# Optimization experiments

Hardware: AMD Instinct MI355X
Metric: run time of the kernel (lower is better)

The kernel has to match this reference:

```python
import jax, jax.numpy as jnp
import numpy as np

NC, NM, E = 100000, 50000, 1000000
IN_C, IN_M, HID, OUT = 128, 64, 128, 64


def setup_inputs() -> dict:
    key = jax.random.key(0)
    ks = jax.random.split(key, 24)
    f = lambda k, shp: jax.random.normal(k, shp, dtype=jnp.float32) * 0.05
    inp = {
        'x_customer': f(ks[0], (NC, IN_C)),
        'x_merchant': f(ks[1], (NM, IN_M)),
        'W1cm_l': f(ks[2], (IN_C, HID)), 'W1cm_r': f(ks[3], (IN_M, HID)), 'b1_cm': f(ks[4], (HID,)),
        'W1mc_l': f(ks[5], (IN_M, HID)), 'W1mc_r': f(ks[6], (IN_C, HID)), 'b1_mc': f(ks[7], (HID,)),
        'W2cm_l': f(ks[8], (HID, HID)), 'W2cm_r': f(ks[9], (HID, HID)), 'b2_cm': f(ks[10], (HID,)),
        'W2mc_l': f(ks[11], (HID, HID)), 'W2mc_r': f(ks[12], (HID, HID)), 'b2_mc': f(ks[13], (HID,)),
        'Wout': f(ks[14], (HID, OUT)), 'bout': f(ks[15], (OUT,)),
        'ei_cm_src': jax.random.randint(ks[16], (E,), 0, NC, dtype=jnp.int32),
        'ei_cm_dst': jax.random.randint(ks[17], (E,), 0, NM, dtype=jnp.int32),
        'ei_mc_src': jax.random.randint(ks[18], (E,), 0, NM, dtype=jnp.int32),
        'ei_mc_dst': jax.random.randint(ks[19], (E,), 0, NC, dtype=jnp.int32),
    }
    return inp


def _sage(x_src, x_dst, src, dst, Wl, Wr, b, n_dst):
    # PyG SAGEConv: out = lin_l(mean_{j in N(i)} x_j) + lin_r(x_i)
    msg = x_src[src]                                        # [E, d_src] gather
    s = jax.ops.segment_sum(msg, dst, num_segments=n_dst)   # [n_dst, d_src]
    c = jax.ops.segment_sum(jnp.ones((src.shape[0],), x_src.dtype), dst, num_segments=n_dst)
    agg = s / jnp.maximum(c, 1.0)[:, None]                  # mean aggregation
    return agg @ Wl + b + x_dst @ Wr


def reference(x_customer, x_merchant,
              W1cm_l, W1cm_r, b1_cm, W1mc_l, W1mc_r, b1_mc,
              W2cm_l, W2cm_r, b2_cm, W2mc_l, W2mc_r, b2_mc,
              Wout, bout,
              ei_cm_src, ei_cm_dst, ei_mc_src, ei_mc_dst):
    # Layer 1 (bipartite): customer->merchant and merchant->customer; sum-merge is
    # trivial (one edge type per destination node type), then ReLU.
    h_m = jax.nn.relu(_sage(x_customer, x_merchant, ei_cm_src, ei_cm_dst, W1cm_l, W1cm_r, b1_cm, NM))
    h_c = jax.nn.relu(_sage(x_merchant, x_customer, ei_mc_src, ei_mc_dst, W1mc_l, W1mc_r, b1_mc, NC))
    # Layer 2 (hidden -> hidden)
    h_c2 = _sage(h_m, h_c, ei_mc_src, ei_mc_dst, W2mc_l, W2mc_r, b2_mc, NC)
    # Final linear on 'customer' embeddings
    return h_c2 @ Wout + bout
```

## Files before the change

### kernel.cpp

```cpp
#include <hip/hip_runtime.h>

#define NCUST 100000
#define NMERCH 50000
#define NEDGE 1000000
#define NTOT (NCUST + NMERCH)
#define HID 128
#define INC 128
#define INM 64
#define OUTD 64

#define SHIFT 9
#define BUCKW 512
#define NBUCKET ((NTOT + BUCKW - 1) / BUCKW)
#define EPB 4096
#define EPT (EPB / 256)

typedef __attribute__((ext_vector_type(8))) short s8v;
typedef __attribute__((ext_vector_type(4))) float f32x4;

__device__ __forceinline__ void splitpair(float a, float b, uint& hw, uint& lw) {
    uint ua = __float_as_uint(a), ub = __float_as_uint(b);
    uint ha = ua & 0xFFFF0000u, hb = ub & 0xFFFF0000u;
    hw = hb | (ua >> 16);
    float ra = a - __uint_as_float(ha);
    float rb = b - __uint_as_float(hb);
    lw = (__float_as_uint(rb) & 0xFFFF0000u) | (__float_as_uint(ra) >> 16);
}


__global__ __launch_bounds__(256) void bcount_kernel(const int* __restrict__ cm_dst,
                                                     const int* __restrict__ mc_dst,
                                                     int* __restrict__ bcnt) {
    __shared__ int lh[NBUCKET];
    const int t = threadIdx.x;
    for (int i = t; i < NBUCKET; i += 256) lh[i] = 0;
    __syncthreads();
    const int base = blockIdx.x * EPB;
#pragma unroll
    for (int i = 0; i < EPT; ++i) {
        int idx = base + t + i * 256;
        if (idx < NEDGE) {
            atomicAdd(&lh[cm_dst[idx] >> SHIFT], 1);
        } else if (idx < 2 * NEDGE) {
            atomicAdd(&lh[(NMERCH + mc_dst[idx - NEDGE]) >> SHIFT], 1);
        }
    }
    __syncthreads();
    for (int i = t; i < NBUCKET; i += 256) {
        int c = lh[i];
        if (c > 0) atomicAdd(&bcnt[i], c);
    }
}

__global__ __launch_bounds__(512) void scan_buckets_kernel(const int* __restrict__ bcnt,
                                                           int* __restrict__ bbase,
                                                           int* __restrict__ bcur,
                                                           int* __restrict__ ro) {
    __shared__ int sh[512];
    const int t = threadIdx.x;
    int v = (t < NBUCKET) ? bcnt[t] : 0;
    sh[t] = v;
    __syncthreads();
    for (int off = 1; off < 512; off <<= 1) {
        int x = (t >= off) ? sh[t - off] : 0;
        __syncthreads();
        sh[t] += x;
        __syncthreads();
    }
    if (t < NBUCKET) {
        int e = sh[t] - v;
        bbase[t] = e;
        bcur[t] = e;
    }
    if (t == 0) {
        bbase[NBUCKET] = 2 * NEDGE;
        ro[NTOT] = 2 * NEDGE;
    }
}

__global__ __launch_bounds__(256) void bin_kernel(const int* __restrict__ cm_src,
                                                  const int* __restrict__ cm_dst,
                                                  const int* __restrict__ mc_src,
                                                  const int* __restrict__ mc_dst,
                                                  int* __restrict__ bcur,
                                                  int2* __restrict__ pairs) {
    __shared__ int lhist[NBUCKET];
    __shared__ int lbase[NBUCKET];
    __shared__ int loff[NBUCKET];
    const int t = threadIdx.x;
    for (int i = t; i < NBUCKET; i += 256) { lhist[i] = 0; loff[i] = 0; }
    __syncthreads();
    const int base = blockIdx.x * EPB;
    int k_[EPT], s_[EPT];
#pragma unroll
    for (int i = 0; i < EPT; ++i) {
        int idx = base + t + i * 256;
        int key = -1, src = 0;
        if (idx < NEDGE) {
            key = cm_dst[idx];
            src = cm_src[idx];
        } else if (idx < 2 * NEDGE) {
            key = NMERCH + mc_dst[idx - NEDGE];
            src = mc_src[idx - NEDGE];
        }
        k_[i] = key;
        s_[i] = src;
        if (key >= 0) atomicAdd(&lhist[key >> SHIFT], 1);
    }
    __syncthreads();
    for (int b = t; b < NBUCKET; b += 256) {
        int c = lhist[b];
        if (c > 0) lbase[b] = atomicAdd(&bcur[b], c);
    }
    __syncthreads();
#pragma unroll
    for (int i = 0; i < EPT; ++i) {
        if (k_[i] >= 0) {
            int bk = k_[i] >> SHIFT;
            int p = lbase[bk] + atomicAdd(&loff[bk], 1);
            pairs[p] = make_int2(k_[i], s_[i]);
        }
    }
}

__global__ __launch_bounds__(512) void fillb_kernel(const int2* __restrict__ pairs,
                                                    const int* __restrict__ bbase,
                                                    int* __restrict__ ro,
                                                    int* __restrict__ csr) {
    __shared__ int hist[BUCKW];
    __shared__ int cur[BUCKW];
    const int b = blockIdx.x, t = threadIdx.x;
    const int kb = b << SHIFT;
    const int nk = (kb + BUCKW < NTOT) ? BUCKW : (NTOT - kb);
    hist[t] = 0;
    __syncthreads();
    const int start = bbase[b], end = bbase[b + 1];
    for (int i = start + t; i < end; i += 512) atomicAdd(&hist[pairs[i].x - kb], 1);
    __syncthreads();
    int v = hist[t];
    cur[t] = v;
    __syncthreads();
    for (int off = 1; off < 512; off <<= 1) {
        int x = (t >= off) ? cur[t - off] : 0;
        __syncthreads();
        cur[t] += x;
        __syncthreads();
    }
    int pos = start + cur[t] - v;
    if (t < nk) ro[kb + t] = pos;
    cur[t] = pos;
    __syncthreads();
    for (int i = start + t; i < end; i += 512) {
        int2 rec = pairs[i];
        int p = atomicAdd(&cur[rec.x - kb], 1);
        csr[p] = rec.y;
    }
}


__global__ __launch_bounds__(256) void agg_cm_kernel(const float* __restrict__ xc,
                                                     const int* __restrict__ csr,
                                                     const int* __restrict__ ro,
                                                     float* __restrict__ aggm) {
    int node = blockIdx.x * 4 + (threadIdx.x >> 6);
    int lane = threadIdx.x & 63;
    if (node >= NMERCH) return;
    int start = ro[node], end = ro[node + 1];
    float2 a0 = {0.f, 0.f}, a1 = {0.f, 0.f}, a2 = {0.f, 0.f}, a3 = {0.f, 0.f};
    int e = start;
    for (; e + 4 <= end; e += 4) {
        int s0 = csr[e], s1 = csr[e + 1], s2 = csr[e + 2], s3 = csr[e + 3];
        float2 v0 = *(const float2*)(xc + (size_t)s0 * INC + lane * 2);
        float2 v1 = *(const float2*)(xc + (size_t)s1 * INC + lane * 2);
        float2 v2 = *(const float2*)(xc + (size_t)s2 * INC + lane * 2);
        float2 v3 = *(const float2*)(xc + (size_t)s3 * INC + lane * 2);
        a0.x += v0.x; a0.y += v0.y;
        a1.x += v1.x; a1.y += v1.y;
        a2.x += v2.x; a2.y += v2.y;
        a3.x += v3.x; a3.y += v3.y;
    }
    for (; e < end; ++e) {
        int s0 = csr[e];
        float2 v0 = *(const float2*)(xc + (size_t)s0 * INC + lane * 2);
        a0.x += v0.x; a0.y += v0.y;
    }
    int deg = end - start;
    float cnt = (float)(deg > 0 ? deg : 1);
    float2 o;
    o.x = (a0.x + a1.x + a2.x + a3.x) / cnt;
    o.y = (a0.y + a1.y + a2.y + a3.y) / cnt;
    *(float2*)(aggm + (size_t)node * HID + lane * 2) = o;
}

__global__ __launch_bounds__(256) void agg_mc_kernel(const float* __restrict__ xm,
                                                     const float* __restrict__ t2p,
                                                     const int* __restrict__ csr,
                                                     const int* __restrict__ ro,
                                                     float* __restrict__ agg_c,
                                                     float* __restrict__ aggT2) {
    int node = blockIdx.x * 4 + (threadIdx.x >> 6);
    int lane = threadIdx.x & 63;
    if (node >= NCUST) return;
    int start = ro[NMERCH + node], end = ro[NMERCH + node + 1];
    float a0 = 0.f, a1 = 0.f, a2 = 0.f, a3 = 0.f;
    float h0 = 0.f, h1 = 0.f, h2 = 0.f, h3 = 0.f;
    int e = start;
    for (; e + 4 <= end; e += 4) {
        int s0 = csr[e], s1 = csr[e + 1], s2 = csr[e + 2], s3 = csr[e + 3];
        a0 += xm[(size_t)s0 * INM + lane];
        a1 += xm[(size_t)s1 * INM + lane];
        a2 += xm[(size_t)s2 * INM + lane];
        a3 += xm[(size_t)s3 * INM + lane];
        h0 += t2p[(size_t)s0 * OUTD + lane];
        h1 += t2p[(size_t)s1 * OUTD + lane];
        h2 += t2p[(size_t)s2 * OUTD + lane];
        h3 += t2p[(size_t)s3 * OUTD + lane];
    }
    for (; e < end; ++e) {
        int s0 = csr[e];
        a0 += xm[(size_t)s0 * INM + lane];
        h0 += t2p[(size_t)s0 * OUTD + lane];
    }
    int deg = end - start;
    float cnt = (float)(deg > 0 ? deg : 1);
    agg_c[(size_t)node * INM + lane] = (a0 + a1 + a2 + a3) / cnt;
    aggT2[(size_t)node * OUTD + lane] = (h0 + h1 + h2 + h3) / cnt;
}


__global__ __launch_bounds__(64) void small_mm_kernel(const float* __restrict__ Wa,
                                                      const float* __restrict__ Wb,
                                                      float* __restrict__ o) {
    __shared__ float row[128];
    int r = blockIdx.x, j = threadIdx.x;
    for (int k = j; k < 128; k += 64) row[k] = Wa[r * 128 + k];
    __syncthreads();
    float acc = 0.f;
    for (int k = 0; k < 128; ++k) acc = fmaf(row[k], Wb[k * 64 + j], acc);
    o[r * 64 + j] = acc;
}

__global__ void bprime_kernel(const float* __restrict__ b2, const float* __restrict__ Wout,
                              const float* __restrict__ bout, float* __restrict__ bprime) {
    int j = threadIdx.x;
    float acc = bout[j];
    for (int k = 0; k < HID; ++k) acc = fmaf(b2[k], Wout[k * OUTD + j], acc);
    bprime[j] = acc;
}


__global__ __launch_bounds__(256) void wprep_kernel(const float* __restrict__ w0,
                                                    const float* __restrict__ w1,
                                                    const float* __restrict__ w2,
                                                    const float* __restrict__ w3,
                                                    const float* __restrict__ w4,
                                                    const float* __restrict__ w5,
                                                    short* __restrict__ planes) {
    int b = blockIdx.x;
    const float* src;
    int N, kt, hoff, loff;
    if (b < 4)       { src = w0; N = 128; kt = b;      hoff = 0;      loff = 16384; }
    else if (b < 6)  { src = w1; N = 128; kt = b - 4;  hoff = 32768;  loff = 40960; }
    else if (b < 8)  { src = w2; N = 128; kt = b - 6;  hoff = 49152;  loff = 57344; }
    else if (b < 12) { src = w3; N = 128; kt = b - 8;  hoff = 65536;  loff = 81920; }
    else if (b < 16) { src = w4; N = 64;  kt = b - 12; hoff = 98304;  loff = 106496; }
    else             { src = w5; N = 64;  kt = b - 16; hoff = 114688; loff = 122880; }

    for (int slot = threadIdx.x; slot < N * 4; slot += 256) {
        int n = slot % N, kg = slot / N;
        uint hw[4], lw[4];
#pragma unroll
        for (int p = 0; p < 4; ++p) {
            float a = src[(kt * 32 + kg * 8 + 2 * p) * N + n];
            float c = src[(kt * 32 + kg * 8 + 2 * p + 1) * N + n];
            splitpair(a, c, hw[p], lw[p]);
        }
        size_t eoff = (size_t)((kt * 4 + kg) * N + n) * 8;
        *(int4*)&planes[hoff + eoff] = make_int4(hw[0], hw[1], hw[2], hw[3]);
        *(int4*)&planes[loff + eoff] = make_int4(lw[0], lw[1], lw[2], lw[3]);
    }
}


template <int KA, int KB, int NOUT, bool RELU, bool HASBIAS, bool HASADD>
__global__ __launch_bounds__(256) void mfma_gemm(const float* __restrict__ A,
                                                 const float* __restrict__ B,
                                                 const short* __restrict__ WAh,
                                                 const short* __restrict__ WAl,
                                                 const short* __restrict__ WBh,
                                                 const short* __restrict__ WBl,
                                                 const float* __restrict__ bias,
                                                 const float* __restrict__ add,
                                                 float* __restrict__ out, int M) {
    constexpr int NSA = KA / 32, NSB = KB / 32, NS = NSA + NSB;
    constexpr int CBN = NOUT / 32;

    __shared__ int4 AhL[2][512];
    __shared__ int4 AlL[2][512];

    const int t = threadIdx.x;
    const int lane = t & 63;
    const int wv = t >> 6;
    const int wr = wv >> 1;
    const int wc = wv & 1;
    const int rowbase = blockIdx.x * 128;
    const int srow = t >> 1, kh = t & 1;

    float4 pa[4];

    auto gload = [&](int s) {
        const float* src;
        int lda, ks;
        if (s < NSA) { src = A; lda = KA; ks = s * 32; }
        else         { src = B; lda = KB; ks = (s - NSA) * 32; }
        const int grow = rowbase + srow;
        if (grow < M) {
            const float* p = src + (size_t)grow * lda + ks + kh * 16;
            pa[0] = *(const float4*)(p);
            pa[1] = *(const float4*)(p + 4);
            pa[2] = *(const float4*)(p + 8);
            pa[3] = *(const float4*)(p + 12);
        } else {
            pa[0] = pa[1] = pa[2] = pa[3] = make_float4(0.f, 0.f, 0.f, 0.f);
        }
    };

    auto stage = [&](int bb) {
        uint h[8], l[8];
        splitpair(pa[0].x, pa[0].y, h[0], l[0]);
        splitpair(pa[0].z, pa[0].w, h[1], l[1]);
        splitpair(pa[1].x, pa[1].y, h[2], l[2]);
        splitpair(pa[1].z, pa[1].w, h[3], l[3]);
        splitpair(pa[2].x, pa[2].y, h[4], l[4]);
        splitpair(pa[2].z, pa[2].w, h[5], l[5]);
        splitpair(pa[3].x, pa[3].y, h[6], l[6]);
        splitpair(pa[3].z, pa[3].w, h[7], l[7]);
        const int base0 = (2 * kh) * 128 + srow;
        const int base1 = base0 + 128;
        AhL[bb][base0] = make_int4(h[0], h[1], h[2], h[3]);
        AhL[bb][base1] = make_int4(h[4], h[5], h[6], h[7]);
        AlL[bb][base0] = make_int4(l[0], l[1], l[2], l[3]);
        AlL[bb][base1] = make_int4(l[4], l[5], l[6], l[7]);
    };

    f32x4 acc[4][CBN];
#pragma unroll
    for (int rb = 0; rb < 4; ++rb)
#pragma unroll
        for (int cb = 0; cb < CBN; ++cb) acc[rb][cb] = (f32x4){0.f, 0.f, 0.f, 0.f};

    const int kgl = lane >> 4, ln = lane & 15;

    gload(0);
    stage(0);
    for (int s = 0; s < NS; ++s) {
        if (s + 1 < NS) gload(s + 1);
        __syncthreads();
        const short *wph_, *wpl_;
        int wb;
        if (s < NSA) { wph_ = WAh; wpl_ = WAl; wb = s; }
        else         { wph_ = WBh; wpl_ = WBl; wb = s - NSA; }
        const s8v* wph = (const s8v*)wph_;
        const s8v* wpl = (const s8v*)wpl_;
        s8v bh[CBN], bl[CBN];
#pragma unroll
        for (int cb = 0; cb < CBN; ++cb) {
            int n = wc * (NOUT / 2) + cb * 16 + ln;
            int idx = (wb * 4 + kgl) * NOUT + n;
            bh[cb] = wph[idx];
            bl[cb] = wpl[idx];
        }
        const int bb = s & 1;
#pragma unroll
        for (int rb = 0; rb < 4; ++rb) {
            int row = wr * 64 + rb * 16 + ln;
            s8v ah = *(const s8v*)&AhL[bb][kgl * 128 + row];
            s8v al = *(const s8v*)&AlL[bb][kgl * 128 + row];
#pragma unroll
            for (int cb = 0; cb < CBN; ++cb) {
                acc[rb][cb] = __builtin_amdgcn_mfma_f32_16x16x32_bf16(ah, bh[cb], acc[rb][cb], 0, 0, 0);
                acc[rb][cb] = __builtin_amdgcn_mfma_f32_16x16x32_bf16(ah, bl[cb], acc[rb][cb], 0, 0, 0);
                acc[rb][cb] = __builtin_amdgcn_mfma_f32_16x16x32_bf16(al, bh[cb], acc[rb][cb], 0, 0, 0);
            }
        }
        if (s + 1 < NS) stage((s + 1) & 1);
    }

#pragma unroll
    for (int cb = 0; cb < CBN; ++cb) {
        int col = wc * (NOUT / 2) + cb * 16 + ln;
        float bv = HASBIAS ? bias[col] : 0.f;
#pragma unroll
        for (int rb = 0; rb < 4; ++rb) {
#pragma unroll
            for (int i = 0; i < 4; ++i) {
                int grow = rowbase + wr * 64 + rb * 16 + kgl * 4 + i;
                if (grow < M) {
                    float o = acc[rb][cb][i] + bv;
                    if (HASADD) o += add[(size_t)grow * NOUT + col];
                    if (RELU) o = fmaxf(o, 0.f);
                    out[(size_t)grow * NOUT + col] = o;
                }
            }
        }
    }
}


extern "C" void kernel_launch(void* const* d_in, const int* in_sizes, int n_in,
                              void* d_out, int out_size, void* d_ws, size_t ws_size,
                              hipStream_t stream) {
    const float* x_c    = (const float*)d_in[0];
    const float* x_m    = (const float*)d_in[1];
    const float* W1cm_l = (const float*)d_in[2];
    const float* W1cm_r = (const float*)d_in[3];
    const float* b1_cm  = (const float*)d_in[4];
    const float* W1mc_l = (const float*)d_in[5];
    const float* W1mc_r = (const float*)d_in[6];
    const float* b1_mc  = (const float*)d_in[7];
    const float* W2mc_l = (const float*)d_in[11];
    const float* W2mc_r = (const float*)d_in[12];
    const float* b2_mc  = (const float*)d_in[13];
    const float* Wout   = (const float*)d_in[14];
    const float* bout   = (const float*)d_in[15];
    const int* cm_src   = (const int*)d_in[16];
    const int* cm_dst   = (const int*)d_in[17];
    const int* mc_src   = (const int*)d_in[18];
    const int* mc_dst   = (const int*)d_in[19];
    float* out = (float*)d_out;

    char* ws = (char*)d_ws;
    size_t off = 0;
    auto bump = [&](size_t bytes) -> char* {
        off = (off + 255) & ~(size_t)255;
        char* p = ws + off;
        off += bytes;
        return p;
    };
    int* ro       = (int*)bump((size_t)(NTOT + 1) * 4);
    int* bcnt     = (int*)bump((size_t)NBUCKET * 4);
    int* bbase    = (int*)bump((size_t)(NBUCKET + 1) * 4);
    int* bcur     = (int*)bump((size_t)NBUCKET * 4);
    int* csr      = (int*)bump((size_t)2 * NEDGE * 4);
    float* bufA   = (float*)bump((size_t)NCUST * HID * 4);
    float* t2p    = (float*)bump((size_t)NMERCH * OUTD * 4);
    float* agg_c  = (float*)bump((size_t)NCUST * INM * 4);
    float* aggT2  = (float*)bump((size_t)NCUST * OUTD * 4);
    float* h_c    = (float*)bump((size_t)NCUST * HID * 4);
    float* w2ro   = (float*)bump((size_t)HID * OUTD * 4);
    float* w2lo   = (float*)bump((size_t)HID * OUTD * 4);
    float* bpr    = (float*)bump((size_t)OUTD * 4);
    short* planes = (short*)bump((size_t)131072 * 2);

    float* t_agg_m = bufA;
    float* h_m     = bufA + (size_t)NMERCH * HID;
    int2* pairs    = (int2*)h_c;

    small_mm_kernel<<<128, 64, 0, stream>>>(W2mc_r, Wout, w2ro);
    small_mm_kernel<<<128, 64, 0, stream>>>(W2mc_l, Wout, w2lo);
    bprime_kernel<<<1, 64, 0, stream>>>(b2_mc, Wout, bout, bpr);
    wprep_kernel<<<20, 256, 0, stream>>>(W1cm_l, W1cm_r, W1mc_l, W1mc_r, w2ro, w2lo, planes);

    hipMemsetAsync(bcnt, 0, (size_t)NBUCKET * 4, stream);
    bcount_kernel<<<(2 * NEDGE + EPB - 1) / EPB, 256, 0, stream>>>(cm_dst, mc_dst, bcnt);
    scan_buckets_kernel<<<1, 512, 0, stream>>>(bcnt, bbase, bcur, ro);
    bin_kernel<<<(2 * NEDGE + EPB - 1) / EPB, 256, 0, stream>>>(cm_src, cm_dst, mc_src, mc_dst,
                                                                bcur, pairs);
    fillb_kernel<<<NBUCKET, 512, 0, stream>>>(pairs, bbase, ro, csr);

    short* Pcml_h = planes;           short* Pcml_l = planes + 16384;
    short* Pcmr_h = planes + 32768;   short* Pcmr_l = planes + 40960;
    short* Pmcl_h = planes + 49152;   short* Pmcl_l = planes + 57344;
    short* Pmcr_h = planes + 65536;   short* Pmcr_l = planes + 81920;
    short* Pro_h  = planes + 98304;   short* Pro_l  = planes + 106496;
    short* Plo_h  = planes + 114688;  short* Plo_l  = planes + 122880;

    agg_cm_kernel<<<NMERCH / 4, 256, 0, stream>>>(x_c, csr, ro, t_agg_m);
    mfma_gemm<128, 64, 128, true, true, false><<<(NMERCH + 127) / 128, 256, 0, stream>>>(
        t_agg_m, x_m, Pcml_h, Pcml_l, Pcmr_h, Pcmr_l, b1_cm, nullptr, h_m, NMERCH);

    mfma_gemm<128, 0, 64, false, false, false><<<(NMERCH + 127) / 128, 256, 0, stream>>>(
        h_m, nullptr, Plo_h, Plo_l, nullptr, nullptr, nullptr, nullptr, t2p, NMERCH);

    agg_mc_kernel<<<NCUST / 4, 256, 0, stream>>>(x_m, t2p, csr, ro, agg_c, aggT2);

    mfma_gemm<64, 128, 128, true, true, false><<<(NCUST + 127) / 128, 256, 0, stream>>>(
        agg_c, x_c, Pmcl_h, Pmcl_l, Pmcr_h, Pmcr_l, b1_mc, nullptr, h_c, NCUST);

    mfma_gemm<128, 0, 64, false, true, true><<<(NCUST + 127) / 128, 256, 0, stream>>>(
        h_c, nullptr, Pro_h, Pro_l, nullptr, nullptr, bpr, aggT2, out, NCUST);
}
```

Baseline: 462.1 us.

## Gather bf16 copies of node features and interleave merchant rows for aggregation

Converts x_customer to bf16 and packs x_merchant together with the projected layer-2 merchant features into one interleaved 128-wide bf16 row per merchant. Both aggregation kernels then gather half the bytes per edge, and the merchant-to-customer gather reads one contiguous row instead of two separate arrays. This adds two conversion kernels and a bf16 output path in the GEMM. The price is bf16 rounding of the gathered inputs, which may loosen accuracy compared with the previous split-precision fp32 path.

New measurement: 428.8 us. 7.2% less time.

```diff
diff --git a/kernel.cpp b/kernel.cpp
--- a/kernel.cpp
+++ b/kernel.cpp
@@ -25,6 +25,46 @@
     float ra = a - __uint_as_float(ha);
     float rb = b - __uint_as_float(hb);
     lw = (__float_as_uint(rb) & 0xFFFF0000u) | (__float_as_uint(ra) >> 16);
+}
+
+__device__ __forceinline__ uint f2bfbits(float x) {
+    uint u = __float_as_uint(x);
+    return (u + 0x7FFFu + ((u >> 16) & 1u)) >> 16;
+}
+__device__ __forceinline__ uint packbf(float a, float b) {
+    return f2bfbits(a) | (f2bfbits(b) << 16);
+}
+__device__ __forceinline__ float bflo(uint v) { return __uint_as_float(v << 16); }
+__device__ __forceinline__ float bfhi(uint v) { return __uint_as_float(v & 0xFFFF0000u); }
+
+
+__global__ __launch_bounds__(256) void tobf_kernel(const float* __restrict__ in,
+                                                   ushort* __restrict__ outp, int n8) {
+    int i = blockIdx.x * 256 + threadIdx.x;
+    if (i >= n8) return;
+    const float4* p = (const float4*)in + (size_t)i * 2;
+    float4 u = p[0], v = p[1];
+    uint4 w;
+    w.x = packbf(u.x, u.y);
+    w.y = packbf(u.z, u.w);
+    w.z = packbf(v.x, v.y);
+    w.w = packbf(v.z, v.w);
+    ((uint4*)outp)[i] = w;
+}
+
+__global__ __launch_bounds__(256) void xmpack_kernel(const float* __restrict__ xm,
+                                                     ushort* __restrict__ mcpk) {
+    int tid = blockIdx.x * 256 + threadIdx.x;
+    if (tid >= NMERCH * 8) return;
+    int n = tid >> 3, c = (tid & 7) * 8;
+    const float* p = xm + (size_t)n * INM + c;
+    float4 u = *(const float4*)p, v = *(const float4*)(p + 4);
+    uint4 w;
+    w.x = packbf(u.x, u.y);
+    w.y = packbf(u.z, u.w);
+    w.z = packbf(v.x, v.y);
+    w.w = packbf(v.z, v.w);
+    *(uint4*)(mcpk + (size_t)n * 128 + c) = w;
 }
 
 
@@ -158,7 +198,7 @@
 }
 
 
-__global__ __launch_bounds__(256) void agg_cm_kernel(const float* __restrict__ xc,
+__global__ __launch_bounds__(256) void agg_cm_kernel(const ushort* __restrict__ xcb,
                                                      const int* __restrict__ csr,
                                                      const int* __restrict__ ro,
                                                      float* __restrict__ aggm) {
@@ -166,34 +206,33 @@
     int lane = threadIdx.x & 63;
     if (node >= NMERCH) return;
     int start = ro[node], end = ro[node + 1];
-    float2 a0 = {0.f, 0.f}, a1 = {0.f, 0.f}, a2 = {0.f, 0.f}, a3 = {0.f, 0.f};
+    float a0 = 0.f, b0 = 0.f, a1 = 0.f, b1 = 0.f;
+    float a2 = 0.f, b2 = 0.f, a3 = 0.f, b3 = 0.f;
     int e = start;
     for (; e + 4 <= end; e += 4) {
         int s0 = csr[e], s1 = csr[e + 1], s2 = csr[e + 2], s3 = csr[e + 3];
-        float2 v0 = *(const float2*)(xc + (size_t)s0 * INC + lane * 2);
-        float2 v1 = *(const float2*)(xc + (size_t)s1 * INC + lane * 2);
-        float2 v2 = *(const float2*)(xc + (size_t)s2 * INC + lane * 2);
-        float2 v3 = *(const float2*)(xc + (size_t)s3 * INC + lane * 2);
-        a0.x += v0.x; a0.y += v0.y;
-        a1.x += v1.x; a1.y += v1.y;
-        a2.x += v2.x; a2.y += v2.y;
-        a3.x += v3.x; a3.y += v3.y;
+        uint v0 = *(const uint*)(xcb + (size_t)s0 * INC + lane * 2);
+        uint v1 = *(const uint*)(xcb + (size_t)s1 * INC + lane * 2);
+        uint v2 = *(const uint*)(xcb + (size_t)s2 * INC + lane * 2);
+        uint v3 = *(const uint*)(xcb + (size_t)s3 * INC + lane * 2);
+        a0 += bflo(v0); b0 += bfhi(v0);
+        a1 += bflo(v1); b1 += bfhi(v1);
+        a2 += bflo(v2); b2 += bfhi(v2);
+        a3 += bflo(v3); b3 += bfhi(v3);
     }
     for (; e < end; ++e) {
-        int s0 = csr[e];
-        float2 v0 = *(const float2*)(xc + (size_t)s0 * INC + lane * 2);
-        a0.x += v0.x; a0.y += v0.y;
+        uint v0 = *(const uint*)(xcb + (size_t)csr[e] * INC + lane * 2);
+        a0 += bflo(v0); b0 += bfhi(v0);
     }
     int deg = end - start;
     float cnt = (float)(deg > 0 ? deg : 1);
     float2 o;
-    o.x = (a0.x + a1.x + a2.x + a3.x) / cnt;
-    o.y = (a0.y + a1.y + a2.y + a3.y) / cnt;
+    o.x = (a0 + a1 + a2 + a3) / cnt;
+    o.y = (b0 + b1 + b2 + b3) / cnt;
     *(float2*)(aggm + (size_t)node * HID + lane * 2) = o;
 }
 
-__global__ __launch_bounds__(256) void agg_mc_kernel(const float* __restrict__ xm,
-                                                     const float* __restrict__ t2p,
+__global__ __launch_bounds__(256) void agg_mc_kernel(const ushort* __restrict__ mcpk,
                                                      const int* __restrict__ csr,
                                                      const int* __restrict__ ro,
                                                      float* __restrict__ agg_c,
@@ -202,29 +241,34 @@
     int lane = threadIdx.x & 63;
     if (node >= NCUST) return;
     int start = ro[NMERCH + node], end = ro[NMERCH + node + 1];
-    float a0 = 0.f, a1 = 0.f, a2 = 0.f, a3 = 0.f;
-    float h0 = 0.f, h1 = 0.f, h2 = 0.f, h3 = 0.f;
+    float a0 = 0.f, b0 = 0.f, a1 = 0.f, b1 = 0.f;
+    float a2 = 0.f, b2 = 0.f, a3 = 0.f, b3 = 0.f;
     int e = start;
     for (; e + 4 <= end; e += 4) {
         int s0 = csr[e], s1 = csr[e + 1], s2 = csr[e + 2], s3 = csr[e + 3];
-        a0 += xm[(size_t)s0 * INM + lane];
-        a1 += xm[(size_t)s1 * INM + lane];
-        a2 += xm[(size_t)s2 * INM + lane];
-        a3 += xm[(size_t)s3 * INM + lane];
-        h0 += t2p[(size_t)s0 * OUTD + lane];
-        h1 += t2p[(size_t)s1 * OUTD + lane];
-        h2 += t2p[(size_t)s2 * OUTD + lane];
-        h3 += t2p[(size_t)s3 * OUTD + lane];
+        uint v0 = *(const uint*)(mcpk + (size_t)s0 * 128 + lane * 2);
+        uint v1 = *(const uint*)(mcpk + (size_t)s1 * 128 + lane * 2);
+        uint v2 = *(const uint*)(mcpk + (size_t)s2 * 128 + lane * 2);
+        uint v3 = *(const uint*)(mcpk + (size_t)s3 * 128 + lane * 2);
+        a0 += bflo(v0); b0 += bfhi(v0);
+        a1 += bflo(v1); b1 += bfhi(v1);
+        a2 += bflo(v2); b2 += bfhi(v2);
+        a3 += bflo(v3); b3 += bfhi(v3);
     }
     for (; e < end; ++e) {
-        int s0 = csr[e];
-        a0 += xm[(size_t)s0 * INM + lane];
-        h0 += t2p[(size_t)s0 * OUTD + lane];
+        uint v0 = *(const uint*)(mcpk + (size_t)csr[e] * 128 + lane * 2);
+        a0 += bflo(v0); b0 += bfhi(v0);
     }
     int deg = end - start;
     float cnt = (float)(deg > 0 ? deg : 1);
-    agg_c[(size_t)node * INM + lane] = (a0 + a1 + a2 + a3) / cnt;
-    aggT2[(size_t)node * OUTD + lane] = (h0 + h1 + h2 + h3) / cnt;
+    float2 o;
+    o.x = (a0 + a1 + a2 + a3) / cnt;
+    o.y = (b0 + b1 + b2 + b3) / cnt;
+    if (lane < 32) {
+        *(float2*)(agg_c + (size_t)node * INM + lane * 2) = o;
+    } else {
+        *(float2*)(aggT2 + (size_t)node * OUTD + (lane - 32) * 2) = o;
+    }
 }
 
 
@@ -282,7 +326,7 @@
 }
 
 
-template <int KA, int KB, int NOUT, bool RELU, bool HASBIAS, bool HASADD>
+template <int KA, int KB, int NOUT, bool RELU, bool HASBIAS, bool HASADD, bool OUTBF16>
 __global__ __launch_bounds__(256) void mfma_gemm(const float* __restrict__ A,
                                                  const float* __restrict__ B,
                                                  const short* __restrict__ WAh,
@@ -291,7 +335,9 @@
                                                  const short* __restrict__ WBl,
                                                  const float* __restrict__ bias,
                                                  const float* __restrict__ add,
-                                                 float* __restrict__ out, int M) {
+                                                 float* __restrict__ out,
+                                                 ushort* __restrict__ outb, int oldd,
+                                                 int M) {
     constexpr int NSA = KA / 32, NSB = KB / 32, NS = NSA + NSB;
     constexpr int CBN = NOUT / 32;
 
@@ -399,7 +445,11 @@
                     float o = acc[rb][cb][i] + bv;
                     if (HASADD) o += add[(size_t)grow * NOUT + col];
                     if (RELU) o = fmaxf(o, 0.f);
-                    out[(size_t)grow * NOUT + col] = o;
+                    if (OUTBF16) {
+                        outb[(size_t)grow * oldd + col] = (ushort)f2bfbits(o);
+                    } else {
+                        out[(size_t)grow * NOUT + col] = o;
+                    }
                 }
             }
         }
@@ -443,7 +493,6 @@
     int* bcur     = (int*)bump((size_t)NBUCKET * 4);
     int* csr      = (int*)bump((size_t)2 * NEDGE * 4);
     float* bufA   = (float*)bump((size_t)NCUST * HID * 4);
-    float* t2p    = (float*)bump((size_t)NMERCH * OUTD * 4);
     float* agg_c  = (float*)bump((size_t)NCUST * INM * 4);
     float* aggT2  = (float*)bump((size_t)NCUST * OUTD * 4);
     float* h_c    = (float*)bump((size_t)NCUST * HID * 4);
@@ -451,6 +500,8 @@
     float* w2lo   = (float*)bump((size_t)HID * OUTD * 4);
     float* bpr    = (float*)bump((size_t)OUTD * 4);
     short* planes = (short*)bump((size_t)131072 * 2);
+    ushort* xcb   = (ushort*)bump((size_t)NCUST * INC * 2);
+    ushort* mcpk  = (ushort*)bump((size_t)NMERCH * 128 * 2);
 
     float* t_agg_m = bufA;
     float* h_m     = bufA + (size_t)NMERCH * HID;
@@ -460,6 +511,8 @@
     small_mm_kernel<<<128, 64, 0, stream>>>(W2mc_l, Wout, w2lo);
     bprime_kernel<<<1, 64, 0, stream>>>(b2_mc, Wout, bout, bpr);
     wprep_kernel<<<20, 256, 0, stream>>>(W1cm_l, W1cm_r, W1mc_l, W1mc_r, w2ro, w2lo, planes);
+    tobf_kernel<<<(NCUST * INC / 8 + 255) / 256, 256, 0, stream>>>(x_c, xcb, NCUST * INC / 8);
+    xmpack_kernel<<<(NMERCH * 8 + 255) / 256, 256, 0, stream>>>(x_m, mcpk);
 
     hipMemsetAsync(bcnt, 0, (size_t)NBUCKET * 4, stream);
     bcount_kernel<<<(2 * NEDGE + EPB - 1) / EPB, 256, 0, stream>>>(cm_dst, mc_dst, bcnt);
@@ -475,18 +528,19 @@
     short* Pro_h  = planes + 98304;   short* Pro_l  = planes + 106496;
     short* Plo_h  = planes + 114688;  short* Plo_l  = planes + 122880;
 
-    agg_cm_kernel<<<NMERCH / 4, 256, 0, stream>>>(x_c, csr, ro, t_agg_m);
-    mfma_gemm<128, 64, 128, true, true, false><<<(NMERCH + 127) / 128, 256, 0, stream>>>(
-        t_agg_m, x_m, Pcml_h, Pcml_l, Pcmr_h, Pcmr_l, b1_cm, nullptr, h_m, NMERCH);
-
-    mfma_gemm<128, 0, 64, false, false, false><<<(NMERCH + 127) / 128, 256, 0, stream>>>(
-        h_m, nullptr, Plo_h, Plo_l, nullptr, nullptr, nullptr, nullptr, t2p, NMERCH);
-
-    agg_mc_kernel<<<NCUST / 4, 256, 0, stream>>>(x_m, t2p, csr, ro, agg_c, aggT2);
-
-    mfma_gemm<64, 128, 128, true, true, false><<<(NCUST + 127) / 128, 256, 0, stream>>>(
-        agg_c, x_c, Pmcl_h, Pmcl_l, Pmcr_h, Pmcr_l, b1_mc, nullptr, h_c, NCUST);
-
-    mfma_gemm<128, 0, 64, false, true, true><<<(NCUST + 127) / 128, 256, 0, stream>>>(
-        h_c, nullptr, Pro_h, Pro_l, nullptr, nullptr, bpr, aggT2, out, NCUST);
-}
+    agg_cm_kernel<<<NMERCH / 4, 256, 0, stream>>>(xcb, csr, ro, t_agg_m);
+    mfma_gemm<128, 64, 128, true, true, false, false><<<(NMERCH + 127) / 128, 256, 0, stream>>>(
+        t_agg_m, x_m, Pcml_h, Pcml_l, Pcmr_h, Pcmr_l, b1_cm, nullptr, h_m, nullptr, 0, NMERCH);
+
+    mfma_gemm<128, 0, 64, false, false, false, true><<<(NMERCH + 127) / 128, 256, 0, stream>>>(
+        h_m, nullptr, Plo_h, Plo_l, nullptr, nullptr, nullptr, nullptr, nullptr,
+        mcpk + 64, 128, NMERCH);
+
+    agg_mc_kernel<<<NCUST / 4, 256, 0, stream>>>(mcpk, csr, ro, agg_c, aggT2);
+
+    mfma_gemm<64, 128, 128, true, true, false, false><<<(NCUST + 127) / 128, 256, 0, stream>>>(
+        agg_c, x_c, Pmcl_h, Pmcl_l, Pmcr_h, Pmcr_l, b1_mc, nullptr, h_c, nullptr, 0, NCUST);
+
+    mfma_gemm<128, 0, 64, false, true, true, false><<<(NCUST + 127) / 128, 256, 0, stream>>>(
+        h_c, nullptr, Pro_h, Pro_l, nullptr, nullptr, bpr, aggT2, out, nullptr, 0, NCUST);
+}
```
